# Kernel optimization log

Hardware: AMD Instinct MI355X
Metric: run time of the kernel (lower is better)

Reference implementation:

```python
import jax, jax.numpy as jnp
import numpy as np
import math

B, T = 8, 1024
IN_DIMS = 1024
OUT_DIMS = 1024
NUM_CODES = 1024
NUM_CODEBOOKS = 8


def setup_inputs() -> dict:
    key = jax.random.key(0)
    k1, k2, k3, k4, k5 = jax.random.split(key, 5)
    x = jax.random.normal(k1, (B, T, IN_DIMS), dtype=jnp.float32)
    target = jax.random.randint(k2, (B, T, NUM_CODEBOOKS), 0, NUM_CODES, dtype=jnp.int64)
    # params, init per reset_params()
    codebook = jax.random.normal(k3, (NUM_CODES, NUM_CODEBOOKS, OUT_DIMS), dtype=jnp.float32) / math.sqrt(OUT_DIMS * NUM_CODEBOOKS)
    proj_w = jax.random.normal(k4, (NUM_CODEBOOKS * NUM_CODES, IN_DIMS), dtype=jnp.float32) / math.sqrt(IN_DIMS)
    proj_b = jnp.zeros((NUM_CODEBOOKS * NUM_CODES,), dtype=jnp.float32)
    wproj_w = jax.random.normal(k5, (NUM_CODEBOOKS, IN_DIMS), dtype=jnp.float32) / math.sqrt(IN_DIMS)
    return {"x": x, "target": target, "codebook": codebook,
            "proj_w": proj_w, "proj_b": proj_b, "wproj_w": wproj_w}


def reference(x, target, codebook, proj_w, proj_b, wproj_w):
    # xp: (B, T, K, C)
    xp = (jnp.einsum('btd,nd->btn', x, proj_w) + proj_b).reshape(B, T, NUM_CODEBOOKS, NUM_CODES)
    # xw: (B, T, K) softmax codebook weights
    xw = jax.nn.softmax(jnp.einsum('btd,kd->btk', x, wproj_w), axis=-1)
    # gather codebook embeddings under no_grad: codebook[target, arange(K)] -> (B, T, K, D)
    cb_inds = jnp.arange(NUM_CODEBOOKS)
    codebook_embs = jax.lax.stop_gradient(codebook[target, cb_inds])
    # per-element cross entropy, reduction='none' -> (B, T, K)
    logp = jax.nn.log_softmax(xp, axis=-1)
    x_loss = -jnp.take_along_axis(logp, target[..., None], axis=-1)[..., 0]
    # softmax-weighted sum over codebooks -> (B, T, D)
    emb = jnp.einsum('btkd,btk->btd', codebook_embs, xw)
    return emb, x_loss
```

## Files before the change

### kernel.cpp

```cpp
#include <hip/hip_runtime.h>
#include <hip/hip_bf16.h>
#include <math.h>

#define MTOT   8192
#define KDIM   1024
#define NCODES 1024
#define NCB    8
#define NTOT   8192
#define ODIM   1024

typedef __attribute__((ext_vector_type(8))) short  bf16x8;
typedef __attribute__((ext_vector_type(4))) float  f32x4;

__device__ __forceinline__ ushort f2bf(float f) {
  union { float f; unsigned u; } v; v.f = f;
  unsigned u = v.u;
  unsigned r = (u + 0x7fffu + ((u >> 16) & 1u)) >> 16;
  return (ushort)r;
}

__device__ __forceinline__ void gload16(const void* g, void* l) {
  __builtin_amdgcn_global_load_lds(
      (const __attribute__((address_space(1))) void*)g,
      (__attribute__((address_space(3))) void*)l,
      16, 0, 0);
}

__global__ void cvt_bf16_kernel(const float* __restrict__ in,
                                ushort* __restrict__ out) {
  int i = blockIdx.x * blockDim.x + threadIdx.x;
  float4 v = ((const float4*)in)[i];
  ushort4 o;
  o.x = f2bf(v.x); o.y = f2bf(v.y); o.z = f2bf(v.z); o.w = f2bf(v.w);
  ((ushort4*)out)[i] = o;
}


__device__ __forceinline__ void chunk_dec(int c, int& srcA, int& srcB) {
  const int q  = c >> 6;
  const int sq = q >> 1;
  const int ct = q & 1;
  const int r4 = (c >> 2) & 15;
  const int cb = (((c & 3) ^ ((c >> 3) & 3)) << 4);
  const int rtA = (sq & 3) + ((sq >> 2) << 3);
  const int rtB = (sq & 1) + ((sq >> 1) << 2);
  srcA = ((rtA << 4) + r4) * (KDIM * 2) + ct * 64 + cb;
  srcB = ((rtB << 4) + r4) * (KDIM * 2) + ct * 64 + cb;
}

#define STAGE_A(T, H) do { \
    const int ao_ = (((T) & 15) * 128 + (H) * 131072); \
    char* ld_ = ldsA_st + ((T) & 1) * 32768 + (H) * 16384; \
    gload16(Ag + (size_t)(srcA0 + ao_), ld_); \
    gload16(Ag + (size_t)(srcA1 + ao_), ld_ + 8192); \
  } while(0)
#define STAGE_B(T, H) do { \
    const int bo_ = (((T) >> 4) * 524288 + ((T) & 15) * 128 + (H) * 65536); \
    char* ld_ = ldsB_st + ((T) & 1) * 32768 + (H) * 16384; \
    gload16(Bg + (size_t)(srcB0 + bo_), ld_); \
    gload16(Bg + (size_t)(srcB1 + bo_), ld_ + 8192); \
  } while(0)

#define LDA_Q(P, MH, AR) do { \
    _Pragma("unroll") for (int m_ = 0; m_ < 4; ++m_) \
    _Pragma("unroll") for (int k_ = 0; k_ < 2; ++k_) \
      AR[m_][k_] = *(const bf16x8*)(ldsA_rd + (P)*32768 + (MH)*16384 + m_*2048 + k_*1024); \
  } while(0)
#define LDB_Q(P, NH, BR) do { \
    _Pragma("unroll") for (int n_ = 0; n_ < 2; ++n_) \
    _Pragma("unroll") for (int k_ = 0; k_ < 2; ++k_) \
      BR[n_][k_] = *(const bf16x8*)(ldsB_rd + (P)*32768 + (NH)*16384 + n_*2048 + k_*1024); \
  } while(0)
#define MM_Q(MH, NH, AR, BR) do { \
    _Pragma("unroll") for (int k_ = 0; k_ < 2; ++k_) \
    _Pragma("unroll") for (int m_ = 0; m_ < 4; ++m_) \
    _Pragma("unroll") for (int n_ = 0; n_ < 2; ++n_) \
      acc[(MH)*4+m_][(NH)*2+n_] = __builtin_amdgcn_mfma_f32_16x16x32_bf16( \
          AR[m_][k_], BR[n_][k_], acc[(MH)*4+m_][(NH)*2+n_], 0, 0, 0); \
  } while(0)

#define FLUSH(SEG) do { \
    const int colb_ = (SEG) * 256 + wc * 64; \
    float bias_n[4]; \
    _Pragma("unroll") for (int n_ = 0; n_ < 4; ++n_) \
      bias_n[n_] = bias[kcb * 1024 + colb_ + n_ * 16 + c15]; \
    _Pragma("unroll") for (int m_ = 0; m_ < 8; ++m_) { \
      _Pragma("unroll") for (int j_ = 0; j_ < 4; ++j_) { \
        const int rl_ = wr * 128 + m_ * 16 + g * 4 + j_; \
        const int tc_ = tgtcol[rl_]; \
        float s_ = 0.f; \
        _Pragma("unroll") for (int n_ = 0; n_ < 4; ++n_) { \
          const float v_ = acc[m_][n_][j_] + bias_n[n_]; \
          if (colb_ + n_ * 16 + c15 == tc_) tgtval[rl_] = v_; \
          s_ += __expf(v_); \
        } \
        _Pragma("unroll") for (int o_ = 1; o_ < 16; o_ <<= 1) \
          s_ += __shfl_xor(s_, o_); \
        if (c15 == 0) redS[wc * 256 + rl_] = s_; \
      } \
    } \
    asm volatile("s_waitcnt lgkmcnt(0)" ::: "memory"); \
    asm volatile("s_barrier" ::: "memory"); \
    if (tid < 256) \
      S_acc += redS[tid] + redS[tid + 256] + redS[tid + 512] + redS[tid + 768]; \
    _Pragma("unroll") for (int m_ = 0; m_ < 8; ++m_) \
      _Pragma("unroll") for (int n_ = 0; n_ < 4; ++n_) \
        acc[m_][n_] = (f32x4){0.f, 0.f, 0.f, 0.f}; \
  } while(0)

__global__ __launch_bounds__(512, 2)
void ce_gemm_kernel(const ushort* __restrict__ Abf,
                    const ushort* __restrict__ Bbf,
                    const float*  __restrict__ bias,
                    const int*    __restrict__ target,
                    float* __restrict__ xloss) {
  extern __shared__ char smem[];
  float* redS   = (float*)(smem + 131072);
  int*   tgtcol = (int*)  (smem + 135168);
  float* tgtval = (float*)(smem + 136192);

  const int tid  = threadIdx.x;
  const int wid  = tid >> 6;
  const int lane = tid & 63;
  const int wr   = wid >> 2;
  const int wc   = wid & 3;
  const int g    = lane >> 4;
  const int c15  = lane & 15;
  const int bidx  = blockIdx.x;
  const int u     = bidx >> 3;
  const int mtile = (bidx & 7) * 4 + (u & 3);
  const int kcb   = u >> 2;

  const int swz = (c15 * 64 + g * 16) ^ ((c15 & 6) << 3);
  const char* ldsA_rd = smem + wr * 8192 + swz;
  const char* ldsB_rd = smem + 65536 + wc * 4096 + swz;
  char* ldsA_st = smem + wid * 1024;
  char* ldsB_st = smem + 65536 + wid * 1024;

  const char* Ag = ((const char*)Abf) + (size_t)mtile * 256 * (KDIM * 2);
  const char* Bg = ((const char*)Bbf) + (size_t)kcb * 2097152;
  int srcA0, srcB0, srcA1, srcB1;
  chunk_dec(tid,       srcA0, srcB0);
  chunk_dec(tid + 512, srcA1, srcB1);

  if (tid < 256)
    tgtcol[tid] = target[(size_t)(mtile * 256 + tid) * NCB + kcb];

  f32x4 acc[8][4];
#pragma unroll
  for (int m = 0; m < 8; ++m)
#pragma unroll
    for (int n = 0; n < 4; ++n)
      acc[m][n] = (f32x4){0.f, 0.f, 0.f, 0.f};

  float S_acc = 0.f;
  bf16x8 a0[4][2], a1[4][2], b0[2][2], b1[2][2];

  STAGE_A(0, 0); STAGE_A(0, 1); STAGE_B(0, 0); STAGE_B(0, 1);
  STAGE_A(1, 0); STAGE_B(1, 0); STAGE_B(1, 1);
  asm volatile("s_waitcnt vmcnt(6)" ::: "memory");
  __syncthreads();

#pragma unroll 1
  for (int t = 0; t < 64; ++t) {
    const int P = t & 1;
    LDA_Q(P, 0, a0); LDB_Q(P, 0, b0); LDB_Q(P, 1, b1); LDA_Q(P, 1, a1);
    if (t < 63) STAGE_A(t + 1, 1);
    __builtin_amdgcn_s_setprio(1);
    MM_Q(0, 0, a0, b0);
    MM_Q(0, 1, a0, b1);
    __builtin_amdgcn_s_setprio(0);
    asm volatile("s_barrier" ::: "memory");
    if (t < 62) { STAGE_A(t + 2, 0); STAGE_B(t + 2, 0); STAGE_B(t + 2, 1); }
    __builtin_amdgcn_s_setprio(1);
    MM_Q(1, 1, a1, b1);
    MM_Q(1, 0, a1, b0);
    __builtin_amdgcn_s_setprio(0);
    if (t < 62) { asm volatile("s_waitcnt vmcnt(6)" ::: "memory"); }
    else        { asm volatile("s_waitcnt vmcnt(0)" ::: "memory"); }
    asm volatile("s_barrier" ::: "memory");
    if ((t & 15) == 15) FLUSH(t >> 4);
  }

  __syncthreads();
  if (tid < 256) {
    const int row = mtile * 256 + tid;
    xloss[(size_t)row * NCB + kcb] = __logf(S_acc) - tgtval[tid];
  }
}

__global__ void emb_kernel(const float* __restrict__ x,
                           const int*   __restrict__ target,
                           const float* __restrict__ cb,
                           const float* __restrict__ wproj,
                           float* __restrict__ emb_out,
                           ushort* __restrict__ xbf) {
  const int bt   = blockIdx.x;
  const int tid  = threadIdx.x;
  const int lane = tid & 63;
  const int wid  = tid >> 6;

  const float4 xv = ((const float4*)(x + (size_t)bt * KDIM))[tid];
  ushort4 xo;
  xo.x = f2bf(xv.x); xo.y = f2bf(xv.y); xo.z = f2bf(xv.z); xo.w = f2bf(xv.w);
  ((ushort4*)(xbf + (size_t)bt * KDIM))[tid] = xo;

  float p[8];
#pragma unroll
  for (int k = 0; k < 8; ++k) {
    const float4 wv = ((const float4*)(wproj + k * KDIM))[tid];
    p[k] = xv.x * wv.x + xv.y * wv.y + xv.z * wv.z + xv.w * wv.w;
  }
#pragma unroll
  for (int k = 0; k < 8; ++k)
#pragma unroll
    for (int off = 32; off >= 1; off >>= 1)
      p[k] += __shfl_xor(p[k], off);

  __shared__ float lred[4][8];
  if (lane == 0) {
#pragma unroll
    for (int k = 0; k < 8; ++k) lred[wid][k] = p[k];
  }
  __syncthreads();

  float logit[8], mx = -1e30f;
#pragma unroll
  for (int k = 0; k < 8; ++k) {
    logit[k] = lred[0][k] + lred[1][k] + lred[2][k] + lred[3][k];
    mx = fmaxf(mx, logit[k]);
  }
  float w[8], den = 0.f;
#pragma unroll
  for (int k = 0; k < 8; ++k) { w[k] = __expf(logit[k] - mx); den += w[k]; }
  const float inv = 1.f / den;

  float4 acc = make_float4(0.f, 0.f, 0.f, 0.f);
#pragma unroll
  for (int k = 0; k < 8; ++k) {
    const int t = target[bt * NCB + k];
    const float4 cv = ((const float4*)(cb + ((size_t)t * NCB + k) * ODIM))[tid];
    const float wk = w[k] * inv;
    acc.x += wk * cv.x; acc.y += wk * cv.y; acc.z += wk * cv.z; acc.w += wk * cv.w;
  }
  ((float4*)(emb_out + (size_t)bt * ODIM))[tid] = acc;
}

extern "C" void kernel_launch(void* const* d_in, const int* in_sizes, int n_in,
                              void* d_out, int out_size, void* d_ws, size_t ws_size,
                              hipStream_t stream) {
  const float* x        = (const float*)d_in[0];
  const int*   target   = (const int*)  d_in[1];
  const float* codebook = (const float*)d_in[2];
  const float* proj_w   = (const float*)d_in[3];
  const float* proj_b   = (const float*)d_in[4];
  const float* wproj_w  = (const float*)d_in[5];

  float* out       = (float*)d_out;
  float* emb_out   = out;
  float* xloss_out = out + (size_t)MTOT * ODIM;

  char* ws = (char*)d_ws;
  ushort* xbf = (ushort*)ws;
  ushort* wbf = (ushort*)(ws + (size_t)16 * 1024 * 1024);

  hipFuncSetAttribute((const void*)ce_gemm_kernel,
                      hipFuncAttributeMaxDynamicSharedMemorySize, 137216);

  emb_kernel<<<MTOT, 256, 0, stream>>>(x, target, codebook, wproj_w, emb_out, xbf);
  cvt_bf16_kernel<<<(NTOT * KDIM / 4) / 256, 256, 0, stream>>>(proj_w, wbf);

  ce_gemm_kernel<<<256, 512, 137216, stream>>>(xbf, wbf, proj_b, target, xloss_out);
}
```

Measured before the change: 212.9 us.

## Retile CE GEMM to 256x128 with 4x2 waves and register double-buffered K loop

Restructures the fused cross-entropy GEMM. Each K step now covers a 256x128 output tile instead of 256x256, the 8 waves are arranged 4x2 with 64x64 sub-tiles, and the loop runs 128 K/N steps with LDS fragment reads double-buffered in registers. The LDS footprint drops from about 137KB to 102KB and accumulator registers are halved, so occupancy should rise and latency should be hidden better. In exchange the B tile is reused across fewer rows, there are more iterations each ending in a full vmcnt(0) wait plus barrier, and the per-block softmax flush runs twice as often.

```diff
diff --git a/kernel.cpp b/kernel.cpp
--- a/kernel.cpp
+++ b/kernel.cpp
@@ -36,57 +36,58 @@
 }
 
 
-__device__ __forceinline__ void chunk_dec(int c, int& srcA, int& srcB) {
-  const int q  = c >> 6;
-  const int sq = q >> 1;
-  const int ct = q & 1;
-  const int r4 = (c >> 2) & 15;
-  const int cb = (((c & 3) ^ ((c >> 3) & 3)) << 4);
-  const int rtA = (sq & 3) + ((sq >> 2) << 3);
-  const int rtB = (sq & 1) + ((sq >> 1) << 2);
-  srcA = ((rtA << 4) + r4) * (KDIM * 2) + ct * 64 + cb;
-  srcB = ((rtB << 4) + r4) * (KDIM * 2) + ct * 64 + cb;
-}
-
-#define STAGE_A(T, H) do { \
-    const int ao_ = (((T) & 15) * 128 + (H) * 131072); \
-    char* ld_ = ldsA_st + ((T) & 1) * 32768 + (H) * 16384; \
-    gload16(Ag + (size_t)(srcA0 + ao_), ld_); \
-    gload16(Ag + (size_t)(srcA1 + ao_), ld_ + 8192); \
-  } while(0)
-#define STAGE_B(T, H) do { \
-    const int bo_ = (((T) >> 4) * 524288 + ((T) & 15) * 128 + (H) * 65536); \
-    char* ld_ = ldsB_st + ((T) & 1) * 32768 + (H) * 16384; \
-    gload16(Bg + (size_t)(srcB0 + bo_), ld_); \
-    gload16(Bg + (size_t)(srcB1 + bo_), ld_ + 8192); \
-  } while(0)
-
-#define LDA_Q(P, MH, AR) do { \
-    _Pragma("unroll") for (int m_ = 0; m_ < 4; ++m_) \
-    _Pragma("unroll") for (int k_ = 0; k_ < 2; ++k_) \
-      AR[m_][k_] = *(const bf16x8*)(ldsA_rd + (P)*32768 + (MH)*16384 + m_*2048 + k_*1024); \
-  } while(0)
-#define LDB_Q(P, NH, BR) do { \
-    _Pragma("unroll") for (int n_ = 0; n_ < 2; ++n_) \
-    _Pragma("unroll") for (int k_ = 0; k_ < 2; ++k_) \
-      BR[n_][k_] = *(const bf16x8*)(ldsB_rd + (P)*32768 + (NH)*16384 + n_*2048 + k_*1024); \
-  } while(0)
-#define MM_Q(MH, NH, AR, BR) do { \
+#define SRC_DEC(c) ((((c) >> 7) * 16 + (((c) >> 3) & 15)) * 2048 \
+                    + ((((c) & 7) ^ (((c) >> 3) & 7)) << 4))
+
+#define STAGE(T) do { \
+    const int kt_ = (T) & 15, ns_ = (T) >> 4, P_ = (T) & 1; \
+    const char* as_ = Ag + kt_ * 128; \
+    char* ad_ = ldsA_st + P_ * 32768; \
+    gload16(as_ + srcA0, ad_); \
+    gload16(as_ + srcA1, ad_ + 8192); \
+    gload16(as_ + srcA2, ad_ + 16384); \
+    gload16(as_ + srcA3, ad_ + 24576); \
+    const char* bs_ = Bg + ns_ * 262144 + kt_ * 128; \
+    char* bd_ = ldsB_st + P_ * 16384; \
+    gload16(bs_ + srcA0, bd_); \
+    gload16(bs_ + srcA1, bd_ + 8192); \
+  } while(0)
+
+#define READS(T, AR, BR) do { \
+    const int P_ = (T) & 1; \
+    const char* ab_ = ldsA_rd + P_ * 32768; \
+    const char* bb_ = ldsB_rd + P_ * 16384; \
+    _Pragma("unroll") for (int m_ = 0; m_ < 4; ++m_) { \
+      AR[m_][0] = *(const bf16x8*)(ab_ + m_ * 2048 + ik0); \
+      AR[m_][1] = *(const bf16x8*)(ab_ + m_ * 2048 + ik1); \
+    } \
+    _Pragma("unroll") for (int n_ = 0; n_ < 4; ++n_) { \
+      BR[n_][0] = *(const bf16x8*)(bb_ + n_ * 2048 + ik0); \
+      BR[n_][1] = *(const bf16x8*)(bb_ + n_ * 2048 + ik1); \
+    } \
+  } while(0)
+
+#define MMALL(AR, BR) do { \
     _Pragma("unroll") for (int k_ = 0; k_ < 2; ++k_) \
     _Pragma("unroll") for (int m_ = 0; m_ < 4; ++m_) \
-    _Pragma("unroll") for (int n_ = 0; n_ < 2; ++n_) \
-      acc[(MH)*4+m_][(NH)*2+n_] = __builtin_amdgcn_mfma_f32_16x16x32_bf16( \
-          AR[m_][k_], BR[n_][k_], acc[(MH)*4+m_][(NH)*2+n_], 0, 0, 0); \
-  } while(0)
+    _Pragma("unroll") for (int n_ = 0; n_ < 4; ++n_) \
+      acc[m_][n_] = __builtin_amdgcn_mfma_f32_16x16x32_bf16( \
+          AR[m_][k_], BR[n_][k_], acc[m_][n_], 0, 0, 0); \
+  } while(0)
+
+#define BOUNDARY \
+    asm volatile("s_waitcnt lgkmcnt(0)" ::: "memory"); \
+    asm volatile("s_waitcnt vmcnt(0)" ::: "memory"); \
+    asm volatile("s_barrier" ::: "memory");
 
 #define FLUSH(SEG) do { \
-    const int colb_ = (SEG) * 256 + wc * 64; \
+    const int colb_ = (SEG) * 128 + wc * 64; \
     float bias_n[4]; \
     _Pragma("unroll") for (int n_ = 0; n_ < 4; ++n_) \
       bias_n[n_] = bias[kcb * 1024 + colb_ + n_ * 16 + c15]; \
-    _Pragma("unroll") for (int m_ = 0; m_ < 8; ++m_) { \
+    _Pragma("unroll") for (int m_ = 0; m_ < 4; ++m_) { \
       _Pragma("unroll") for (int j_ = 0; j_ < 4; ++j_) { \
-        const int rl_ = wr * 128 + m_ * 16 + g * 4 + j_; \
+        const int rl_ = wr * 64 + m_ * 16 + g * 4 + j_; \
         const int tc_ = tgtcol[rl_]; \
         float s_ = 0.f; \
         _Pragma("unroll") for (int n_ = 0; n_ < 4; ++n_) { \
@@ -101,9 +102,8 @@
     } \
     asm volatile("s_waitcnt lgkmcnt(0)" ::: "memory"); \
     asm volatile("s_barrier" ::: "memory"); \
-    if (tid < 256) \
-      S_acc += redS[tid] + redS[tid + 256] + redS[tid + 512] + redS[tid + 768]; \
-    _Pragma("unroll") for (int m_ = 0; m_ < 8; ++m_) \
+    if (tid < 256) S_acc += redS[tid] + redS[tid + 256]; \
+    _Pragma("unroll") for (int m_ = 0; m_ < 4; ++m_) \
       _Pragma("unroll") for (int n_ = 0; n_ < 4; ++n_) \
         acc[m_][n_] = (f32x4){0.f, 0.f, 0.f, 0.f}; \
   } while(0)
@@ -115,15 +115,15 @@
                     const int*    __restrict__ target,
                     float* __restrict__ xloss) {
   extern __shared__ char smem[];
-  float* redS   = (float*)(smem + 131072);
-  int*   tgtcol = (int*)  (smem + 135168);
-  float* tgtval = (float*)(smem + 136192);
+  float* redS   = (float*)(smem + 98304);
+  int*   tgtcol = (int*)  (smem + 100352);
+  float* tgtval = (float*)(smem + 101376);
 
   const int tid  = threadIdx.x;
   const int wid  = tid >> 6;
   const int lane = tid & 63;
-  const int wr   = wid >> 2;
-  const int wc   = wid & 3;
+  const int wr   = wid >> 1;
+  const int wc   = wid & 1;
   const int g    = lane >> 4;
   const int c15  = lane & 15;
   const int bidx  = blockIdx.x;
@@ -131,58 +131,65 @@
   const int mtile = (bidx & 7) * 4 + (u & 3);
   const int kcb   = u >> 2;
 
-  const int swz = (c15 * 64 + g * 16) ^ ((c15 & 6) << 3);
-  const char* ldsA_rd = smem + wr * 8192 + swz;
-  const char* ldsB_rd = smem + 65536 + wc * 4096 + swz;
+  const int ik0 = c15 * 128 + ((g ^ (c15 & 7)) << 4);
+  const int ik1 = ik0 ^ 64;
+
+  const char* ldsA_rd = smem + wr * 8192;
+  const char* ldsB_rd = smem + 65536 + wc * 8192;
   char* ldsA_st = smem + wid * 1024;
   char* ldsB_st = smem + 65536 + wid * 1024;
 
-  const char* Ag = ((const char*)Abf) + (size_t)mtile * 256 * (KDIM * 2);
-  const char* Bg = ((const char*)Bbf) + (size_t)kcb * 2097152;
-  int srcA0, srcB0, srcA1, srcB1;
-  chunk_dec(tid,       srcA0, srcB0);
-  chunk_dec(tid + 512, srcA1, srcB1);
+  const char* Ag = ((const char*)Abf) + (size_t)mtile * 256 * 2048;
+  const char* Bg = ((const char*)Bbf) + (size_t)kcb * 1024 * 2048;
+
+  const int srcA0 = SRC_DEC(tid);
+  const int srcA1 = SRC_DEC(tid + 512);
+  const int srcA2 = SRC_DEC(tid + 1024);
+  const int srcA3 = SRC_DEC(tid + 1536);
 
   if (tid < 256)
     tgtcol[tid] = target[(size_t)(mtile * 256 + tid) * NCB + kcb];
 
-  f32x4 acc[8][4];
-#pragma unroll
-  for (int m = 0; m < 8; ++m)
+  f32x4 acc[4][4];
+#pragma unroll
+  for (int m = 0; m < 4; ++m)
 #pragma unroll
     for (int n = 0; n < 4; ++n)
       acc[m][n] = (f32x4){0.f, 0.f, 0.f, 0.f};
 
   float S_acc = 0.f;
-  bf16x8 a0[4][2], a1[4][2], b0[2][2], b1[2][2];
-
-  STAGE_A(0, 0); STAGE_A(0, 1); STAGE_B(0, 0); STAGE_B(0, 1);
-  STAGE_A(1, 0); STAGE_B(1, 0); STAGE_B(1, 1);
-  asm volatile("s_waitcnt vmcnt(6)" ::: "memory");
+  bf16x8 a0[4][2], b0v[4][2], a1[4][2], b1v[4][2];
+
+  STAGE(0); STAGE(1);
+  asm volatile("s_waitcnt vmcnt(0)" ::: "memory");
   __syncthreads();
+  READS(0, a0, b0v);
 
 #pragma unroll 1
-  for (int t = 0; t < 64; ++t) {
-    const int P = t & 1;
-    LDA_Q(P, 0, a0); LDB_Q(P, 0, b0); LDB_Q(P, 1, b1); LDA_Q(P, 1, a1);
-    if (t < 63) STAGE_A(t + 1, 1);
+  for (int di = 0; di < 63; ++di) {
+    const int t = 2 * di;
+    STAGE(t + 2);
+    READS(t + 1, a1, b1v);
     __builtin_amdgcn_s_setprio(1);
-    MM_Q(0, 0, a0, b0);
-    MM_Q(0, 1, a0, b1);
+    MMALL(a0, b0v);
     __builtin_amdgcn_s_setprio(0);
-    asm volatile("s_barrier" ::: "memory");
-    if (t < 62) { STAGE_A(t + 2, 0); STAGE_B(t + 2, 0); STAGE_B(t + 2, 1); }
+    BOUNDARY
+    STAGE(t + 3);
+    READS(t + 2, a0, b0v);
     __builtin_amdgcn_s_setprio(1);
-    MM_Q(1, 1, a1, b1);
-    MM_Q(1, 0, a1, b0);
+    MMALL(a1, b1v);
     __builtin_amdgcn_s_setprio(0);
-    if (t < 62) { asm volatile("s_waitcnt vmcnt(6)" ::: "memory"); }
-    else        { asm volatile("s_waitcnt vmcnt(0)" ::: "memory"); }
-    asm volatile("s_barrier" ::: "memory");
-    if ((t & 15) == 15) FLUSH(t >> 4);
-  }
-
-  __syncthreads();
+    BOUNDARY
+    if ((di & 7) == 7) FLUSH(di >> 3);
+  }
+  READS(127, a1, b1v);
+  __builtin_amdgcn_s_setprio(1);
+  MMALL(a0, b0v);
+  __builtin_amdgcn_s_setprio(0);
+  BOUNDARY
+  MMALL(a1, b1v);
+  FLUSH(7);
+
   if (tid < 256) {
     const int row = mtile * 256 + tid;
     xloss[(size_t)row * NCB + kcb] = __logf(S_acc) - tgtval[tid];
@@ -265,10 +272,10 @@
   ushort* wbf = (ushort*)(ws + (size_t)16 * 1024 * 1024);
 
   hipFuncSetAttribute((const void*)ce_gemm_kernel,
-                      hipFuncAttributeMaxDynamicSharedMemorySize, 137216);
+                      hipFuncAttributeMaxDynamicSharedMemorySize, 102400);
 
   emb_kernel<<<MTOT, 256, 0, stream>>>(x, target, codebook, wproj_w, emb_out, xbf);
   cvt_bf16_kernel<<<(NTOT * KDIM / 4) / 256, 256, 0, stream>>>(proj_w, wbf);
 
-  ce_gemm_kernel<<<256, 512, 137216, stream>>>(xbf, wbf, proj_b, target, xloss_out);
-}
+  ce_gemm_kernel<<<256, 512, 102400, stream>>>(xbf, wbf, proj_b, target, xloss_out);
+}
```

Result: faster. 194.0 us (median of 4 runs) (-8.9%).
